# Optimization experiments

Measured on AMD Instinct MI355X. Metric: run time of the kernel, lower is better.

## Reference

```python
import jax, jax.numpy as jnp
import numpy as np

# ---- config (matches init_kwargs) ----
B, NP, DIM, HEADS, DH, NDIM = 32, 576, 512, 8, 64, 16
N = NP + 1                 # seq len incl cls token = 577
INNER = HEADS * DH         # 512


def setup_inputs() -> dict:
    key = jax.random.key(0)
    ks = jax.random.split(key, 11)
    D2 = 2 * DIM  # bidirectional EMA doubles kernel dim
    return {
        "x": jax.random.normal(ks[0], (B, N, DIM), jnp.float32),
        "W_qk": jax.random.normal(ks[1], (DIM, 2 * INNER), jnp.float32) / np.float32(np.sqrt(DIM)),
        "W_v": jax.random.normal(ks[2], (DIM, INNER), jnp.float32) / np.float32(np.sqrt(DIM)),
        "W_out": jax.random.normal(ks[3], (INNER, DIM), jnp.float32) / np.float32(np.sqrt(INNER)),
        "b_out": jnp.zeros((DIM,), jnp.float32),
        "rel_bias": jax.random.normal(ks[4], (2 * N - 1,), jnp.float32) * 0.02,
        "ema_delta": jax.random.normal(ks[5], (D2, NDIM, 1), jnp.float32),
        "ema_alpha": jax.random.normal(ks[6], (D2, NDIM, 1), jnp.float32),
        "ema_beta": jax.random.normal(ks[7], (D2, NDIM, 1), jnp.float32) * 0.5,
        "ema_gamma": jax.random.normal(ks[8], (D2, NDIM), jnp.float32) * 0.5,
        "ema_omega": jax.random.normal(ks[9], (DIM,), jnp.float32),
    }


def _ema_move(x, delta, alpha, beta, gamma, omega):
    """Bidirectional MultiHeadEMA (MEGA) via FFT convolution. x: (B, L, D)."""
    b, L, d = x.shape
    scale = jnp.asarray(np.sqrt(1.0 / NDIM), x.dtype)
    p = jax.nn.sigmoid(delta)                      # (2D, N, 1)
    q = 1.0 - p * jax.nn.sigmoid(alpha)            # (2D, N, 1), in (0,1)
    vander = jnp.arange(L, dtype=x.dtype)[None, None, :] * jnp.log(q)  # (2D, N, L)
    kern = (p * beta) * jnp.exp(vander)            # (2D, N, L)
    k = jnp.einsum('dnl,dn->dl', kern, gamma * scale)  # (2D, L)
    k1, k2 = k[:d], k[d:]
    # combined bidirectional kernel, length 2L-1
    kk = jnp.pad(k1, ((0, 0), (L - 1, 0))) + jnp.pad(k2[:, ::-1], ((0, 0), (0, L - 1)))
    xt = jnp.pad(x.transpose(0, 2, 1), ((0, 0), (0, 0), (L - 1, 0)))  # (B, D, 2L-1)
    fft_len = 2 * L - 1
    nfft = 2 * fft_len
    out = jnp.fft.irfft(jnp.fft.rfft(xt, n=nfft) * jnp.fft.rfft(kk, n=nfft)[None], n=nfft)
    s = 2 * L - 2
    out = out[..., s:s + L].transpose(0, 2, 1).astype(x.dtype)  # (B, L, D)
    return jax.nn.silu(out + x * omega)


def _rel_pos_bias(rb, seq_len):
    """RelativePositionalBias (MEGA): (2*N-1,) param -> (seq_len, seq_len) bias."""
    max_pos = N
    bvec = rb[max_pos - seq_len: max_pos + seq_len - 1]   # (2*seq_len-1,)
    t = jnp.pad(bvec, (0, seq_len))
    t = jnp.tile(t, seq_len)[:-seq_len].reshape(seq_len, 3 * seq_len - 2)
    r = (2 * seq_len - 1) // 2
    return t[:, r:t.shape[1] - r]


def reference(x, W_qk, W_v, W_out, b_out, rel_bias,
              ema_delta, ema_alpha, ema_beta, ema_gamma, ema_omega):
    b, n, _ = x.shape
    cls_tok = x[:, :1]
    moved = _ema_move(x[:, 1:], ema_delta, ema_alpha, ema_beta, ema_gamma, ema_omega)
    xm = jnp.concatenate([cls_tok, moved], axis=1)        # (B, N, DIM)
    q, k = jnp.split(xm @ W_qk, 2, axis=-1)
    v = xm @ W_v                                          # smooth_v_as_well=True

    def heads(t):
        return t.reshape(b, n, HEADS, DH).transpose(0, 2, 1, 3)  # (B, H, N, DH)

    q, k, v = heads(q), heads(k), heads(v)
    dots = jnp.einsum('bhid,bhjd->bhij', q, k) * (DH ** -0.5)
    attn = jax.nn.softmax(dots, axis=-1)
    attn = attn + _rel_pos_bias(rel_bias, n)[None, None]  # bias added AFTER softmax
    out = jnp.einsum('bhij,bhjd->bhid', attn, v)
    out = out.transpose(0, 2, 1, 3).reshape(b, n, INNER)
    return out @ W_out + b_out
```

## Files before the change

### kernel.cpp

```cpp
#include <hip/hip_runtime.h>

typedef unsigned short ushort;

typedef __bf16 bf16x8 __attribute__((ext_vector_type(8)));
typedef float  f32x4  __attribute__((ext_vector_type(4)));
typedef unsigned short u16x8 __attribute__((ext_vector_type(8)));
typedef unsigned short u16x4 __attribute__((ext_vector_type(4)));
typedef unsigned int   u32x2 __attribute__((ext_vector_type(2)));

static constexpr int BB   = 32;
static constexpr int NN   = 577;
static constexpr int LL   = 576;
static constexpr int DIMC = 512;
static constexpr int BN   = BB * NN;

static constexpr size_t SZ_WQKVT = 1536ull * 512 * 2;
static constexpr size_t SZ_WOUTT = 512ull * 512 * 2;
static constexpr size_t SZ_QK    = (size_t)BN * 1024 * 2;
static constexpr size_t SZ_V     = (size_t)BN * 512 * 2;
static constexpr size_t SZ_VT    = 256ull * 64 * 640 * 2;
static constexpr size_t OFF_WQKVT = 0;
static constexpr size_t OFF_WOUTT = OFF_WQKVT + SZ_WQKVT;
static constexpr size_t OFF_QTAB  = OFF_WOUTT + SZ_WOUTT;
static constexpr size_t OFF_CTAB  = OFF_QTAB + 65536;
static constexpr size_t OFF_QK    = OFF_CTAB + 65536;
static constexpr size_t OFF_V     = OFF_QK + SZ_QK;
static constexpr size_t OFF_REGION= OFF_V + SZ_V;
static constexpr size_t OFF_XM    = OFF_REGION;
static constexpr size_t OFF_VT    = OFF_REGION;
static constexpr size_t OFF_AO    = OFF_REGION + SZ_VT;
static constexpr size_t OFF_ST    = OFF_AO;
static constexpr size_t WS_NEEDED = OFF_AO + SZ_V;

__device__ __forceinline__ ushort bf16bits(float f) {
  unsigned int u = __builtin_bit_cast(unsigned int, f);
  u = (u + 0x7fffu + ((u >> 16) & 1u)) >> 16;
  return (ushort)u;
}
__device__ __forceinline__ float sigmoidf_(float z) { return 1.f / (1.f + __expf(-z)); }
__device__ __forceinline__ float siluf(float z)     { return z / (1.f + __expf(-z)); }

__global__ __launch_bounds__(256) void k_prep(
    const float* __restrict__ delta, const float* __restrict__ alpha,
    const float* __restrict__ beta,  const float* __restrict__ gamma,
    const float* __restrict__ Wqk,   const float* __restrict__ Wv,
    const float* __restrict__ Wout,
    float* __restrict__ qtab, float* __restrict__ ctab,
    ushort* __restrict__ Wqkvt, ushort* __restrict__ Woutt)
{
  int idx = blockIdx.x * 256 + threadIdx.x;
  if (idx < 16384) {
    float p = sigmoidf_(delta[idx]);
    float q = 1.f - p * sigmoidf_(alpha[idx]);
    qtab[idx] = q;
    ctab[idx] = p * beta[idx] * gamma[idx] * 0.25f;
  }
  int i2 = idx - 16384;
  if (i2 >= 0 && i2 < 1536 * 512) {
    int n = i2 >> 9, k = i2 & 511;
    float w = (n < 1024) ? Wqk[k * 1024 + n] : Wv[k * 512 + (n - 1024)];
    Wqkvt[i2] = bf16bits(w);
  }
  int i3 = i2 - 1536 * 512;
  if (i3 >= 0 && i3 < 512 * 512) {
    int n = i3 >> 9, k = i3 & 511;
    Woutt[i3] = bf16bits(Wout[k * 512 + n]);
  }
}


__global__ __launch_bounds__(64) void k_ema_p1(
    const float* __restrict__ x, const float* __restrict__ qtab,
    float* __restrict__ st)
{
  const int gx = blockIdx.x, cy = blockIdx.y, b = blockIdx.z;
  if (gx < 8) {
    const int d = gx * 64 + threadIdx.x;
    float q[16], h[16];
    #pragma unroll
    for (int n = 0; n < 16; ++n) { q[n] = qtab[d*16+n]; h[n] = 0.f; }
    const float* xp = x + ((size_t)b * NN + 1) * DIMC + d;
    const int blo = cy * 9;
    float xn[8];
    #pragma unroll
    for (int u = 0; u < 8; ++u) xn[u] = xp[(blo * 8 + u) * DIMC];
    for (int blk = blo; blk < blo + 9; ++blk) {
      float xv[8];
      #pragma unroll
      for (int u = 0; u < 8; ++u) xv[u] = xn[u];
      if (blk < blo + 8) {
        #pragma unroll
        for (int u = 0; u < 8; ++u) xn[u] = xp[((blk + 1) * 8 + u) * DIMC];
      }
      #pragma unroll
      for (int u = 0; u < 8; ++u) {
        float xx = xv[u];
        #pragma unroll
        for (int n = 0; n < 16; ++n) h[n] = fmaf(q[n], h[n], xx);
      }
    }
    float* sp = st + (((size_t)b * 8 + cy) * 16) * 512 + d;
    #pragma unroll
    for (int n = 0; n < 16; ++n) sp[n * 512] = h[n];
  } else {
    const int d = (gx - 8) * 64 + threadIdx.x;
    float q[16], g[16];
    #pragma unroll
    for (int n = 0; n < 16; ++n) { q[n] = qtab[(d+512)*16+n]; g[n] = 0.f; }
    const float* xp = x + ((size_t)b * NN + 1) * DIMC + d;
    const int blo = (7 - cy) * 9;
    float xn[8];
    #pragma unroll
    for (int u = 0; u < 8; ++u) xn[u] = xp[((blo + 8) * 8 + u) * DIMC];
    for (int blk = blo + 8; blk >= blo; --blk) {
      float xv[8];
      #pragma unroll
      for (int u = 0; u < 8; ++u) xv[u] = xn[u];
      if (blk > blo) {
        #pragma unroll
        for (int u = 0; u < 8; ++u) xn[u] = xp[((blk - 1) * 8 + u) * DIMC];
      }
      #pragma unroll
      for (int u = 7; u >= 0; --u) {
        float xx = xv[u];
        #pragma unroll
        for (int n = 0; n < 16; ++n) g[n] = fmaf(q[n], g[n], xx);
      }
    }
    float* sp = st + (((size_t)(32 + b) * 8 + cy) * 16) * 512 + d;
    #pragma unroll
    for (int n = 0; n < 16; ++n) sp[n * 512] = g[n];
  }
}

__global__ __launch_bounds__(256) void k_ema_mid(
    const float* __restrict__ qtab, float* __restrict__ st)
{
  int idx = blockIdx.x * 256 + threadIdx.x;
  int d = idx & 511;
  int rest = idx >> 9;
  int n = rest & 15;
  int db = rest >> 4;
  int dir = db >> 5;
  float q = qtab[(((size_t)dir << 9) + d) * 16 + n];
  float q2 = q * q, q4 = q2 * q2, q8 = q4 * q4;
  float q16 = q8 * q8, q32 = q16 * q16, q64 = q32 * q32;
  float qL = q64 * q8;
  float h = 0.f;
  float* sp = st + ((size_t)db * 128 + n) * 512 + d;
  #pragma unroll
  for (int c = 0; c < 8; ++c) {
    float tmp = (c < 7) ? sp[c * 8192] : 0.f;
    sp[c * 8192] = h;
    h = fmaf(qL, h, tmp);
  }
}

__global__ __launch_bounds__(64) void k_ema_fuse(
    const float* __restrict__ x, const float* __restrict__ qtab,
    const float* __restrict__ ctab, const float* __restrict__ st,
    const float* __restrict__ omega, ushort* __restrict__ xm)
{
  __shared__ _Float16 yb[72 * 64];
  const int lane = threadIdx.x;
  const int gx = blockIdx.x, cy = blockIdx.y, b = blockIdx.z;
  const int d = gx * 64 + lane;
  const float* xp = x + ((size_t)b * NN + 1 + cy * 72) * DIMC + d;
  {
    float q[16], c[16], g[16];
    const float* sp = st + (((size_t)(32 + b) * 8 + (7 - cy)) * 16) * 512 + d;
    #pragma unroll
    for (int n = 0; n < 16; ++n) {
      q[n] = qtab[(d + 512) * 16 + n];
      c[n] = ctab[(d + 512) * 16 + n];
      g[n] = sp[n * 512];
    }
    float xn[8];
    #pragma unroll
    for (int u = 0; u < 8; ++u) xn[u] = xp[(64 + u) * DIMC];
    for (int blk = 8; blk >= 0; --blk) {
      float xv[8];
      #pragma unroll
      for (int u = 0; u < 8; ++u) xv[u] = xn[u];
      if (blk > 0) {
        #pragma unroll
        for (int u = 0; u < 8; ++u) xn[u] = xp[((blk - 1) * 8 + u) * DIMC];
      }
      #pragma unroll
      for (int u = 7; u >= 0; --u) {
        float xx = xv[u], y = 0.f;
        #pragma unroll
        for (int n = 0; n < 16; ++n) { g[n] = fmaf(q[n], g[n], xx); y = fmaf(c[n], g[n], y); }
        yb[(blk * 8 + u) * 64 + lane] = (_Float16)y;
      }
    }
  }
  __syncthreads();
  {
    float q[16], c[16], h[16];
    const float* sp = st + (((size_t)b * 8 + cy) * 16) * 512 + d;
    #pragma unroll
    for (int n = 0; n < 16; ++n) {
      q[n] = qtab[d * 16 + n];
      c[n] = ctab[d * 16 + n];
      h[n] = sp[n * 512];
    }
    const float om = omega[d];
    ushort* op = xm + ((size_t)b * NN + 1 + cy * 72) * DIMC + d;
    float xn[8];
    #pragma unroll
    for (int u = 0; u < 8; ++u) xn[u] = xp[u * DIMC];
    for (int blk = 0; blk < 9; ++blk) {
      float xv[8];
      #pragma unroll
      for (int u = 0; u < 8; ++u) xv[u] = xn[u];
      if (blk < 8) {
        #pragma unroll
        for (int u = 0; u < 8; ++u) xn[u] = xp[((blk + 1) * 8 + u) * DIMC];
      }
      #pragma unroll
      for (int u = 0; u < 8; ++u) {
        float xx = xv[u], y = 0.f;
        #pragma unroll
        for (int n = 0; n < 16; ++n) { h[n] = fmaf(q[n], h[n], xx); y = fmaf(c[n], h[n], y); }
        float s = y + (float)yb[(blk * 8 + u) * 64 + lane] + xx * om;
        op[(blk * 8 + u) * DIMC] = bf16bits(siluf(s));
      }
    }
  }
  if (cy == 0) {
    size_t e0 = ((size_t)b * NN) * DIMC + d;
    xm[e0] = bf16bits(x[e0]);
  }
}

__global__ __launch_bounds__(256) void k_qkv(
    const ushort* __restrict__ A, const ushort* __restrict__ Bt,
    ushort* __restrict__ qk, ushort* __restrict__ v)
{
  __shared__ alignas(16) ushort lA[128 * 40];
  __shared__ alignas(16) ushort lB[128 * 40];
  const int tid = threadIdx.x, wv = tid >> 6, lane = tid & 63;
  const int quad = lane >> 4, c16 = lane & 15;
  const int fid = blockIdx.y * 12 + blockIdx.x;
  const int xcd = fid & 7, ord = fid >> 3;
  const int wg  = (xcd < 4 ? xcd * 218 : 872 + (xcd - 4) * 217) + ord;
  const int row0 = (wg / 12) * 128, n0 = (wg % 12) * 128;
  const int wm = (wv >> 1) * 64, wn = (wv & 1) * 64;
  f32x4 z4 = {0.f, 0.f, 0.f, 0.f};
  f32x4 acc[4][4];
  #pragma unroll
  for (int mi = 0; mi < 4; ++mi)
    #pragma unroll
    for (int ni = 0; ni < 4; ++ni) acc[mi][ni] = z4;

  for (int kt = 0; kt < 16; ++kt) {
    const int k0 = kt * 32;
    u16x8 sa[2], sb[2];
    #pragma unroll
    for (int it = 0; it < 2; ++it) {
      int ch = it * 256 + tid;
      int r = ch >> 2, cc = ch & 3;
      int grow = row0 + r; if (grow > BN - 1) grow = BN - 1;
      sa[it] = *(const u16x8*)(A + (size_t)grow * 512 + k0 + cc * 8);
      sb[it] = *(const u16x8*)(Bt + (size_t)(n0 + r) * 512 + k0 + cc * 8);
    }
    __syncthreads();
    #pragma unroll
    for (int it = 0; it < 2; ++it) {
      int ch = it * 256 + tid;
      int r = ch >> 2, cc = ch & 3;
      *(u16x8*)(lA + r * 40 + cc * 8) = sa[it];
      *(u16x8*)(lB + r * 40 + cc * 8) = sb[it];
    }
    __syncthreads();
    bf16x8 af[4], bfv[4];
    #pragma unroll
    for (int mi = 0; mi < 4; ++mi)
      af[mi] = *(const bf16x8*)(lA + (wm + mi * 16 + c16) * 40 + quad * 8);
    #pragma unroll
    for (int ni = 0; ni < 4; ++ni)
      bfv[ni] = *(const bf16x8*)(lB + (wn + ni * 16 + c16) * 40 + quad * 8);
    #pragma unroll
    for (int mi = 0; mi < 4; ++mi)
      #pragma unroll
      for (int ni = 0; ni < 4; ++ni)
        acc[mi][ni] = __builtin_amdgcn_mfma_f32_16x16x32_bf16(af[mi], bfv[ni], acc[mi][ni], 0, 0, 0);
  }
  const bool isv = (n0 >= 1024);
  const float osc = (n0 < 512) ? 0.1803368801111f : 1.0f;
  #pragma unroll
  for (int mi = 0; mi < 4; ++mi) {
    #pragma unroll
    for (int r = 0; r < 4; ++r) {
      int grow = row0 + wm + mi * 16 + quad * 4 + r;
      if (grow < BN) {
        #pragma unroll
        for (int ni = 0; ni < 4; ++ni) {
          int col = n0 + wn + ni * 16 + c16;
          ushort vb = bf16bits(acc[mi][ni][r] * osc);
          if (!isv) qk[(size_t)grow * 1024 + col] = vb;
          else      v[(size_t)grow * 512 + (col - 1024)] = vb;
        }
      }
    }
  }
}

__global__ __launch_bounds__(256) void k_vtrans(
    const ushort* __restrict__ v, ushort* __restrict__ vt)
{
  __shared__ alignas(16) ushort lt[64 * 72];
  const int tid = threadIdx.x;
  const int bh = blockIdx.y, b = bh >> 3, h = bh & 7;
  const int j0 = blockIdx.x * 64;
  #pragma unroll
  for (int pass = 0; pass < 2; ++pass) {
    int cch = pass * 256 + tid;
    int jl = cch >> 3, cc = cch & 7;
    int gj = j0 + jl;
    u16x8 val = {0, 0, 0, 0, 0, 0, 0, 0};
    if (gj < 577) val = *(const u16x8*)(v + ((size_t)(b * NN + gj)) * 512 + h * 64 + cc * 8);
    *(u16x8*)(lt + jl * 72 + cc * 8) = val;
  }
  __syncthreads();
  #pragma unroll
  for (int pass = 0; pass < 2; ++pass) {
    int cch = pass * 256 + tid;
    int dh = cch >> 3, jc = cch & 7;
    u16x8 o;
    #pragma unroll
    for (int e = 0; e < 8; ++e) o[e] = lt[(jc * 8 + e) * 72 + dh];
    *(u16x8*)(vt + ((size_t)(bh * 64 + dh)) * 640 + j0 + jc * 8) = o;
  }
}

__global__ __launch_bounds__(256) void k_fattn(
    const ushort* __restrict__ qk, const ushort* __restrict__ vt,
    const float* __restrict__ relb, ushort* __restrict__ ao)
{
  __shared__ alignas(16) ushort lk[64 * 64];
  __shared__ alignas(16) ushort lv[64 * 64];
  __shared__ alignas(16) ushort lp[128 * 64];
  __shared__ ushort lbias16[1280];
  const int tid = threadIdx.x, wv = tid >> 6, lane = tid & 63;
  const int quad = lane >> 4, c16 = lane & 15;
  const int bh = blockIdx.x, b = bh >> 3, h = bh & 7;
  const int i0 = blockIdx.y * 128, wm = wv * 32;
  for (int t = tid; t < 1280; t += 256) {
    int idx = t - 64;
    lbias16[t] = (idx >= 0 && idx < 1153) ? bf16bits(relb[idx]) : (ushort)0;
  }
  bf16x8 aq[2][2];
  #pragma unroll
  for (int ms = 0; ms < 2; ++ms) {
    int gi = i0 + wm + ms * 16 + c16; if (gi > 576) gi = 576;
    const ushort* qp = qk + ((size_t)(b * NN + gi)) * 1024 + h * 64;
    #pragma unroll
    for (int kk = 0; kk < 2; ++kk)
      aq[ms][kk] = *(const bf16x8*)(qp + (kk * 4 + quad) * 8);
  }
  const int s_r = tid >> 3, s_c = tid & 7;
  const ushort* kbase = qk + ((size_t)b * NN) * 1024 + 512 + h * 64 + s_c * 8;
  const ushort* vbase = vt + ((size_t)bh * 64) * 640 + s_c * 8;

  float lsum[2] = {0.f, 0.f};
  f32x4 z4 = {0.f, 0.f, 0.f, 0.f};
  f32x4 accp[2][4], accb[2][4];
  #pragma unroll
  for (int ms = 0; ms < 2; ++ms)
    #pragma unroll
    for (int ns = 0; ns < 4; ++ns) { accp[ms][ns] = z4; accb[ms][ns] = z4; }

  u16x8 sk[2], sv[2];
  #pragma unroll
  for (int it = 0; it < 2; ++it) {
    int r = it * 32 + s_r;
    sk[it] = *(const u16x8*)(kbase + (size_t)r * 1024);
    sv[it] = *(const u16x8*)(vbase + (size_t)r * 640);
  }

  for (int jt = 0; jt < 10; ++jt) {
    __syncthreads();
    #pragma unroll
    for (int it = 0; it < 2; ++it) {
      int r = it * 32 + s_r;
      int pc = (s_c ^ (r & 7)) * 8;
      *(u16x8*)(lk + r * 64 + pc) = sk[it];
      *(u16x8*)(lv + r * 64 + pc) = sv[it];
    }
    __syncthreads();
    if (jt < 9) {
      const int j0n = (jt + 1) * 64;
      #pragma unroll
      for (int it = 0; it < 2; ++it) {
        int r = it * 32 + s_r;
        int gj = j0n + r; if (gj > 576) gj = 576;
        sk[it] = *(const u16x8*)(kbase + (size_t)gj * 1024);
        sv[it] = *(const u16x8*)(vbase + (size_t)r * 640 + j0n);
      }
    }
    #pragma unroll
    for (int ms = 0; ms < 2; ++ms) {
      f32x4 dacc[4] = {z4, z4, z4, z4};
      #pragma unroll
      for (int kk = 0; kk < 2; ++kk) {
        const int ck = kk * 4 + quad;
        #pragma unroll
        for (int ns = 0; ns < 4; ++ns) {
          const int row = ns * 16 + c16;
          bf16x8 bk = *(const bf16x8*)(lk + row * 64 + ((ck ^ (row & 7)) * 8));
          dacc[ns] = __builtin_amdgcn_mfma_f32_16x16x32_bf16(bk, aq[ms][kk], dacc[ns], 0, 0, 0);
        }
      }
      const int irow = wm + ms * 16 + c16;
      const int xr = irow & 7;
      #pragma unroll
      for (int ns = 0; ns < 4; ++ns) {
        float ex[4];
        #pragma unroll
        for (int r = 0; r < 4; ++r) {
          float e = __builtin_amdgcn_exp2f(dacc[ns][r]);
          if (jt == 9 && (ns * 16 + quad * 4 + r) >= 1) e = 0.f;
          ex[r] = e;
        }
        lsum[ms] += (ex[0] + ex[1]) + (ex[2] + ex[3]);
        unsigned int p0 = (unsigned int)bf16bits(ex[0]) | ((unsigned int)bf16bits(ex[1]) << 16);
        unsigned int p1 = (unsigned int)bf16bits(ex[2]) | ((unsigned int)bf16bits(ex[3]) << 16);
        u32x2 pw = {p0, p1};
        const int lc = ns * 2 + (quad >> 1);
        *(u32x2*)(lp + irow * 64 + ((lc ^ xr) * 8) + (quad & 1) * 4) = pw;
      }
    }
    const int j0 = jt * 64;
    #pragma unroll
    for (int kk = 0; kk < 2; ++kk) {
      const int ck = kk * 4 + quad;
      bf16x8 ap[2], ab[2];
      #pragma unroll
      for (int ms = 0; ms < 2; ++ms) {
        const int row = wm + ms * 16 + c16;
        ap[ms] = *(const bf16x8*)(lp + row * 64 + ((ck ^ (row & 7)) * 8));
        u16x8 abu;
        const int base = 64 + 576 + j0 + kk * 32 + quad * 8 - (i0 + row);
        #pragma unroll
        for (int e = 0; e < 8; ++e) abu[e] = lbias16[base + e];
        ab[ms] = __builtin_bit_cast(bf16x8, abu);
      }
      #pragma unroll
      for (int ns = 0; ns < 4; ++ns) {
        const int row = ns * 16 + c16;
        bf16x8 bV = *(const bf16x8*)(lv + row * 64 + ((ck ^ (row & 7)) * 8));
        #pragma unroll
        for (int ms = 0; ms < 2; ++ms) {
          accp[ms][ns] = __builtin_amdgcn_mfma_f32_16x16x32_bf16(ap[ms], bV, accp[ms][ns], 0, 0, 0);
          accb[ms][ns] = __builtin_amdgcn_mfma_f32_16x16x32_bf16(ab[ms], bV, accb[ms][ns], 0, 0, 0);
        }
      }
    }
  }
  float tot[2];
  #pragma unroll
  for (int ms = 0; ms < 2; ++ms) {
    float t = lsum[ms];
    t += __shfl_xor(t, 16);
    t += __shfl_xor(t, 32);
    tot[ms] = t;
  }
  #pragma unroll
  for (int ms = 0; ms < 2; ++ms) {
    #pragma unroll
    for (int r = 0; r < 4; ++r) {
      float li = 1.f / __shfl(tot[ms], quad * 4 + r);
      int ii = i0 + wm + ms * 16 + quad * 4 + r;
      if (ii < 577) {
        #pragma unroll
        for (int ns = 0; ns < 4; ++ns)
          ao[((size_t)(b * NN + ii)) * 512 + h * 64 + ns * 16 + c16] =
              bf16bits(accp[ms][ns][r] * li + accb[ms][ns][r]);
      }
    }
  }
}

__global__ __launch_bounds__(256) void k_out(
    const ushort* __restrict__ A, const ushort* __restrict__ Bt,
    const float* __restrict__ bout, float* __restrict__ out)
{
  __shared__ alignas(16) ushort lA[128 * 40];
  __shared__ alignas(16) ushort lB[128 * 40];
  const int tid = threadIdx.x, wv = tid >> 6, lane = tid & 63;
  const int quad = lane >> 4, c16 = lane & 15;
  const int row0 = blockIdx.y * 128, n0 = blockIdx.x * 128;
  const int wm = (wv >> 1) * 64, wn = (wv & 1) * 64;
  f32x4 z4 = {0.f, 0.f, 0.f, 0.f};
  f32x4 acc[4][4];
  #pragma unroll
  for (int mi = 0; mi < 4; ++mi)
    #pragma unroll
    for (int ni = 0; ni < 4; ++ni) acc[mi][ni] = z4;

  for (int kt = 0; kt < 16; ++kt) {
    const int k0 = kt * 32;
    u16x8 sa[2], sb[2];
    #pragma unroll
    for (int it = 0; it < 2; ++it) {
      int ch = it * 256 + tid;
      int r = ch >> 2, cc = ch & 3;
      int grow = row0 + r; if (grow > BN - 1) grow = BN - 1;
      sa[it] = *(const u16x8*)(A + (size_t)grow * 512 + k0 + cc * 8);
      sb[it] = *(const u16x8*)(Bt + (size_t)(n0 + r) * 512 + k0 + cc * 8);
    }
    __syncthreads();
    #pragma unroll
    for (int it = 0; it < 2; ++it) {
      int ch = it * 256 + tid;
      int r = ch >> 2, cc = ch & 3;
      *(u16x8*)(lA + r * 40 + cc * 8) = sa[it];
      *(u16x8*)(lB + r * 40 + cc * 8) = sb[it];
    }
    __syncthreads();
    bf16x8 af[4], bfv[4];
    #pragma unroll
    for (int mi = 0; mi < 4; ++mi)
      af[mi] = *(const bf16x8*)(lA + (wm + mi * 16 + c16) * 40 + quad * 8);
    #pragma unroll
    for (int ni = 0; ni < 4; ++ni)
      bfv[ni] = *(const bf16x8*)(lB + (wn + ni * 16 + c16) * 40 + quad * 8);
    #pragma unroll
    for (int mi = 0; mi < 4; ++mi)
      #pragma unroll
      for (int ni = 0; ni < 4; ++ni)
        acc[mi][ni] = __builtin_amdgcn_mfma_f32_16x16x32_bf16(af[mi], bfv[ni], acc[mi][ni], 0, 0, 0);
  }
  #pragma unroll
  for (int mi = 0; mi < 4; ++mi) {
    #pragma unroll
    for (int r = 0; r < 4; ++r) {
      int grow = row0 + wm + mi * 16 + quad * 4 + r;
      if (grow < BN) {
        #pragma unroll
        for (int ni = 0; ni < 4; ++ni) {
          int col = n0 + wn + ni * 16 + c16;
          out[(size_t)grow * 512 + col] = acc[mi][ni][r] + bout[col];
        }
      }
    }
  }
}

extern "C" void kernel_launch(void* const* d_in, const int* in_sizes, int n_in,
                              void* d_out, int out_size, void* d_ws, size_t ws_size,
                              hipStream_t stream) {
  (void)in_sizes; (void)n_in; (void)out_size;
  if (ws_size < WS_NEEDED) return;
  const float* x    = (const float*)d_in[0];
  const float* Wqk  = (const float*)d_in[1];
  const float* Wv   = (const float*)d_in[2];
  const float* Wout = (const float*)d_in[3];
  const float* bout = (const float*)d_in[4];
  const float* relb = (const float*)d_in[5];
  const float* edel = (const float*)d_in[6];
  const float* ealp = (const float*)d_in[7];
  const float* ebet = (const float*)d_in[8];
  const float* egam = (const float*)d_in[9];
  const float* eome = (const float*)d_in[10];

  char* ws = (char*)d_ws;
  ushort* Wqkvt = (ushort*)(ws + OFF_WQKVT);
  ushort* Woutt = (ushort*)(ws + OFF_WOUTT);
  float*  qtab  = (float*)(ws + OFF_QTAB);
  float*  ctab  = (float*)(ws + OFF_CTAB);
  ushort* qkb   = (ushort*)(ws + OFF_QK);
  ushort* vb    = (ushort*)(ws + OFF_V);
  ushort* xm    = (ushort*)(ws + OFF_XM);
  ushort* vtb   = (ushort*)(ws + OFF_VT);
  ushort* aob   = (ushort*)(ws + OFF_AO);
  float*  stf   = (float*)(ws + OFF_ST);
  float*  outp  = (float*)d_out;

  k_prep<<<dim3(4160), dim3(256), 0, stream>>>(edel, ealp, ebet, egam, Wqk, Wv, Wout,
                                               qtab, ctab, Wqkvt, Woutt);
  k_ema_p1<<<dim3(16, 7, 32), dim3(64), 0, stream>>>(x, qtab, stf);
  k_ema_mid<<<dim3(2048), dim3(256), 0, stream>>>(qtab, stf);
  k_ema_fuse<<<dim3(8, 8, 32), dim3(64), 0, stream>>>(x, qtab, ctab, stf, eome, xm);
  k_qkv<<<dim3(12, 145), dim3(256), 0, stream>>>(xm, Wqkvt, qkb, vb);
  k_vtrans<<<dim3(10, 256), dim3(256), 0, stream>>>(vb, vtb);
  k_fattn<<<dim3(256, 5), dim3(256), 0, stream>>>(qkb, vtb, relb, aob);
  k_out<<<dim3(4, 145), dim3(256), 0, stream>>>(aob, Woutt, bout, outp);
}
```

Before: 306.4 us.

## Use direct global-to-LDS loads with XOR swizzle in projection GEMMs; pack bf16 with perm

The QKV and output projection GEMMs now stage tiles with global_load_lds, writing directly from global memory into shared memory instead of passing through registers. The LDS layout drops its 40-element padding for a 32-wide layout with an XOR swizzle to avoid bank conflicts. The attention kernel packs pairs of bf16 values with a single byte-permute instruction. Loads are still not double-buffered, so a barrier still separates each load from the compute that uses it. The change relies on the swizzle addressing being correct for both the write and the read side.

Result: faster. 299.8 us (-2.2%).

```diff
diff --git a/kernel.cpp b/kernel.cpp
--- a/kernel.cpp
+++ b/kernel.cpp
@@ -37,8 +37,20 @@
   u = (u + 0x7fffu + ((u >> 16) & 1u)) >> 16;
   return (ushort)u;
 }
+__device__ __forceinline__ unsigned int bf16pk(float lo, float hi) {
+  unsigned int u0 = __builtin_bit_cast(unsigned int, lo);
+  unsigned int u1 = __builtin_bit_cast(unsigned int, hi);
+  unsigned int a0 = u0 + 0x7fffu + ((u0 >> 16) & 1u);
+  unsigned int a1 = u1 + 0x7fffu + ((u1 >> 16) & 1u);
+  return __builtin_amdgcn_perm(a1, a0, 0x07060302);
+}
 __device__ __forceinline__ float sigmoidf_(float z) { return 1.f / (1.f + __expf(-z)); }
 __device__ __forceinline__ float siluf(float z)     { return z / (1.f + __expf(-z)); }
+__device__ __forceinline__ void gload16(const ushort* g, ushort* l) {
+  __builtin_amdgcn_global_load_lds(
+      (const __attribute__((address_space(1))) unsigned int*)g,
+      (__attribute__((address_space(3))) unsigned int*)l, 16, 0, 0);
+}
 
 __global__ __launch_bounds__(256) void k_prep(
     const float* __restrict__ delta, const float* __restrict__ alpha,
@@ -238,8 +250,8 @@
     const ushort* __restrict__ A, const ushort* __restrict__ Bt,
     ushort* __restrict__ qk, ushort* __restrict__ v)
 {
-  __shared__ alignas(16) ushort lA[128 * 40];
-  __shared__ alignas(16) ushort lB[128 * 40];
+  __shared__ alignas(16) ushort lA[128 * 32];
+  __shared__ alignas(16) ushort lB[128 * 32];
   const int tid = threadIdx.x, wv = tid >> 6, lane = tid & 63;
   const int quad = lane >> 4, c16 = lane & 15;
   const int fid = blockIdx.y * 12 + blockIdx.x;
@@ -247,6 +259,16 @@
   const int wg  = (xcd < 4 ? xcd * 218 : 872 + (xcd - 4) * 217) + ord;
   const int row0 = (wg / 12) * 128, n0 = (wg % 12) * 128;
   const int wm = (wv >> 1) * 64, wn = (wv & 1) * 64;
+  const int sr  = wv * 32 + (lane >> 2);
+  const int scs = ((lane & 3) ^ (sr & 3)) * 8;
+  int ga[2], gb[2];
+  #pragma unroll
+  for (int s = 0; s < 2; ++s) {
+    int r = row0 + sr + s * 16; if (r > BN - 1) r = BN - 1;
+    ga[s] = r;
+    gb[s] = n0 + sr + s * 16;
+  }
+  const int xread = (quad ^ (c16 & 3)) * 8;
   f32x4 z4 = {0.f, 0.f, 0.f, 0.f};
   f32x4 acc[4][4];
   #pragma unroll
@@ -256,31 +278,20 @@
 
   for (int kt = 0; kt < 16; ++kt) {
     const int k0 = kt * 32;
-    u16x8 sa[2], sb[2];
-    #pragma unroll
-    for (int it = 0; it < 2; ++it) {
-      int ch = it * 256 + tid;
-      int r = ch >> 2, cc = ch & 3;
-      int grow = row0 + r; if (grow > BN - 1) grow = BN - 1;
-      sa[it] = *(const u16x8*)(A + (size_t)grow * 512 + k0 + cc * 8);
-      sb[it] = *(const u16x8*)(Bt + (size_t)(n0 + r) * 512 + k0 + cc * 8);
-    }
     __syncthreads();
     #pragma unroll
-    for (int it = 0; it < 2; ++it) {
-      int ch = it * 256 + tid;
-      int r = ch >> 2, cc = ch & 3;
-      *(u16x8*)(lA + r * 40 + cc * 8) = sa[it];
-      *(u16x8*)(lB + r * 40 + cc * 8) = sb[it];
+    for (int s = 0; s < 2; ++s) {
+      gload16(A  + (size_t)ga[s] * 512 + k0 + scs, lA + (wv * 32 + s * 16) * 32);
+      gload16(Bt + (size_t)gb[s] * 512 + k0 + scs, lB + (wv * 32 + s * 16) * 32);
     }
     __syncthreads();
     bf16x8 af[4], bfv[4];
     #pragma unroll
     for (int mi = 0; mi < 4; ++mi)
-      af[mi] = *(const bf16x8*)(lA + (wm + mi * 16 + c16) * 40 + quad * 8);
+      af[mi] = *(const bf16x8*)(lA + (wm + mi * 16 + c16) * 32 + xread);
     #pragma unroll
     for (int ni = 0; ni < 4; ++ni)
-      bfv[ni] = *(const bf16x8*)(lB + (wn + ni * 16 + c16) * 40 + quad * 8);
+      bfv[ni] = *(const bf16x8*)(lB + (wn + ni * 16 + c16) * 32 + xread);
     #pragma unroll
     for (int mi = 0; mi < 4; ++mi)
       #pragma unroll
@@ -425,9 +436,7 @@
           ex[r] = e;
         }
         lsum[ms] += (ex[0] + ex[1]) + (ex[2] + ex[3]);
-        unsigned int p0 = (unsigned int)bf16bits(ex[0]) | ((unsigned int)bf16bits(ex[1]) << 16);
-        unsigned int p1 = (unsigned int)bf16bits(ex[2]) | ((unsigned int)bf16bits(ex[3]) << 16);
-        u32x2 pw = {p0, p1};
+        u32x2 pw = { bf16pk(ex[0], ex[1]), bf16pk(ex[2], ex[3]) };
         const int lc = ns * 2 + (quad >> 1);
         *(u32x2*)(lp + irow * 64 + ((lc ^ xr) * 8) + (quad & 1) * 4) = pw;
       }
@@ -487,12 +496,22 @@
     const ushort* __restrict__ A, const ushort* __restrict__ Bt,
     const float* __restrict__ bout, float* __restrict__ out)
 {
-  __shared__ alignas(16) ushort lA[128 * 40];
-  __shared__ alignas(16) ushort lB[128 * 40];
+  __shared__ alignas(16) ushort lA[128 * 32];
+  __shared__ alignas(16) ushort lB[128 * 32];
   const int tid = threadIdx.x, wv = tid >> 6, lane = tid & 63;
   const int quad = lane >> 4, c16 = lane & 15;
   const int row0 = blockIdx.y * 128, n0 = blockIdx.x * 128;
   const int wm = (wv >> 1) * 64, wn = (wv & 1) * 64;
+  const int sr  = wv * 32 + (lane >> 2);
+  const int scs = ((lane & 3) ^ (sr & 3)) * 8;
+  int ga[2], gb[2];
+  #pragma unroll
+  for (int s = 0; s < 2; ++s) {
+    int r = row0 + sr + s * 16; if (r > BN - 1) r = BN - 1;
+    ga[s] = r;
+    gb[s] = n0 + sr + s * 16;
+  }
+  const int xread = (quad ^ (c16 & 3)) * 8;
   f32x4 z4 = {0.f, 0.f, 0.f, 0.f};
   f32x4 acc[4][4];
   #pragma unroll
@@ -502,31 +521,20 @@
 
   for (int kt = 0; kt < 16; ++kt) {
     const int k0 = kt * 32;
-    u16x8 sa[2], sb[2];
-    #pragma unroll
-    for (int it = 0; it < 2; ++it) {
-      int ch = it * 256 + tid;
-      int r = ch >> 2, cc = ch & 3;
-      int grow = row0 + r; if (grow > BN - 1) grow = BN - 1;
-      sa[it] = *(const u16x8*)(A + (size_t)grow * 512 + k0 + cc * 8);
-      sb[it] = *(const u16x8*)(Bt + (size_t)(n0 + r) * 512 + k0 + cc * 8);
-    }
     __syncthreads();
     #pragma unroll
-    for (int it = 0; it < 2; ++it) {
-      int ch = it * 256 + tid;
-      int r = ch >> 2, cc = ch & 3;
-      *(u16x8*)(lA + r * 40 + cc * 8) = sa[it];
-      *(u16x8*)(lB + r * 40 + cc * 8) = sb[it];
+    for (int s = 0; s < 2; ++s) {
+      gload16(A  + (size_t)ga[s] * 512 + k0 + scs, lA + (wv * 32 + s * 16) * 32);
+      gload16(Bt + (size_t)gb[s] * 512 + k0 + scs, lB + (wv * 32 + s * 16) * 32);
     }
     __syncthreads();
     bf16x8 af[4], bfv[4];
     #pragma unroll
     for (int mi = 0; mi < 4; ++mi)
-      af[mi] = *(const bf16x8*)(lA + (wm + mi * 16 + c16) * 40 + quad * 8);
+      af[mi] = *(const bf16x8*)(lA + (wm + mi * 16 + c16) * 32 + xread);
     #pragma unroll
     for (int ni = 0; ni < 4; ++ni)
-      bfv[ni] = *(const bf16x8*)(lB + (wn + ni * 16 + c16) * 40 + quad * 8);
+      bfv[ni] = *(const bf16x8*)(lB + (wn + ni * 16 + c16) * 32 + xread);
     #pragma unroll
     for (int mi = 0; mi < 4; ++mi)
       #pragma unroll
```
